# Kernel optimization log

Measured on AMD Instinct MI355X. Metric: run time of the kernel, lower is better.

Reference implementation:

```python
import jax, jax.numpy as jnp
import numpy as np

N_NODES = 100000
N_EDGES = 3200000
D_IN = 128
D_HID = 16
N_CLS = 2


def gcn_conv(x, edge_index, W, b, n_nodes):
    """PyG GCNConv (normalize=True, add_self_loops=True, bias=True)."""
    h = x @ W  # [N, out]
    loop = jnp.arange(n_nodes, dtype=edge_index.dtype)
    src = jnp.concatenate([edge_index[0], loop])
    dst = jnp.concatenate([edge_index[1], loop])
    deg = jax.ops.segment_sum(jnp.ones_like(dst, dtype=h.dtype), dst, num_segments=n_nodes)
    dinv = jnp.where(deg > 0, jax.lax.rsqrt(deg), jnp.zeros_like(deg))
    norm = dinv[src] * dinv[dst]  # [E+N]
    msg = h[src] * norm[:, None]  # gather + scale
    out = jax.ops.segment_sum(msg, dst, num_segments=n_nodes)  # scatter-add
    return out + b


def setup_inputs() -> dict:
    key = jax.random.key(0)
    k1, k2, k3, k4, k5 = jax.random.split(key, 5)
    x = jax.random.normal(k1, (N_NODES, D_IN), dtype=jnp.float32)
    edge_index = jax.random.randint(k2, (2, N_EDGES), 0, N_NODES, dtype=jnp.int64)
    # Glorot-style init for GCNConv weights, zeros for bias (PyG default)
    W1 = jax.random.normal(k3, (D_IN, D_HID), dtype=jnp.float32) * (1.0 / np.sqrt(D_IN))
    b1 = jnp.zeros((D_HID,), dtype=jnp.float32)
    W2 = jax.random.normal(k4, (D_HID, N_CLS), dtype=jnp.float32) * (1.0 / np.sqrt(D_HID))
    b2 = jnp.zeros((N_CLS,), dtype=jnp.float32)
    return {"x": x, "edge_index": edge_index, "W1": W1, "b1": b1, "W2": W2, "b2": b2}


def reference(x, edge_index, W1, b1, W2, b2):
    n = x.shape[0]
    h = gcn_conv(x, edge_index, W1, b1, n)
    h = jax.nn.relu(h)
    # dropout is identity in eval mode
    h = gcn_conv(h, edge_index, W2, b2, n)
    return jax.nn.log_softmax(h, axis=1)
```

## Files before the change

kernel.cpp:

```cpp
#include <hip/hip_runtime.h>
#include <hip/hip_bf16.h>
#include <hip/hip_fp16.h>

#define D_IN  128
#define D_HID 16
#define N_CLS 2
#define NPB   256
#define MAXB  512
#define TILE  4096
#define XROW  136

#define FE 0

typedef short bf16x8 __attribute__((ext_vector_type(8)));
typedef float f32x4  __attribute__((ext_vector_type(4)));

__device__ __forceinline__ unsigned short f2bf(float f) {
    unsigned int u = __float_as_uint(f);
    u += 0x7FFFu + ((u >> 16) & 1u);
    return (unsigned short)(u >> 16);
}

template<bool I64>
__device__ __forceinline__ int lde(const void* p, size_t i) {
    if constexpr (I64) return (int)((const long long*)p)[i];
    else               return ((const int*)p)[i];
}

__global__ void k_detect(const int* __restrict__ ev, int* __restrict__ flags) {
    __shared__ int sE;
    if (threadIdx.x == 0) sE = 0;
    __syncthreads();
    if (ev[2 * threadIdx.x + 1] != 0) atomicOr(&sE, 1);
    __syncthreads();
    if (threadIdx.x == 0) flags[FE] = sE ? 0 : 1;
}

__global__ __launch_bounds__(MAXB) void k_init(const int* __restrict__ ev, int* __restrict__ flags,
                                               unsigned int* __restrict__ gcur, int cap) {
    __shared__ int sE;
    int tid = threadIdx.x;
    if (tid == 0) sE = 0;
    __syncthreads();
    if (tid < 256 && ev[2 * tid + 1] != 0) atomicOr(&sE, 1);
    gcur[tid] = (unsigned int)(tid * cap);
    __syncthreads();
    if (tid == 0) flags[FE] = sE ? 0 : 1;
}

template<bool I64>
__device__ __forceinline__ void part_body(
        const void* __restrict__ ei, unsigned int* __restrict__ gcur,
        unsigned int* __restrict__ staged, int E, int cap,
        unsigned int* sbuf, unsigned short* bbuf,
        int* hist, int* lbase, int* gb, int* wsum) {
    int tid = threadIdx.x;
    int t0 = blockIdx.x * TILE;

    hist[tid] = 0;
    __syncthreads();

    int myB[8]; unsigned int myP[8]; int myR[8];
#pragma unroll
    for (int k = 0; k < 8; ++k) {
        int e = t0 + k * 512 + tid;
        if (e < E) {
            int s = lde<I64>(ei, (size_t)e);
            int d = lde<I64>(ei, (size_t)E + e);
            int b = d >> 8;
            myB[k] = b;
            myP[k] = ((unsigned int)s << 8) | (unsigned int)(d & 255);
            myR[k] = atomicAdd(&hist[b], 1);
        } else myB[k] = -1;
    }
    __syncthreads();

    int v = hist[tid];
    int lane = tid & 63, wv = tid >> 6;
    int s = v;
#pragma unroll
    for (int m = 1; m < 64; m <<= 1) {
        int t = __shfl_up(s, m, 64);
        if (lane >= m) s += t;
    }
    if (lane == 63) wsum[wv] = s;
    __syncthreads();
    int woff = 0;
#pragma unroll
    for (int w = 0; w < 8; ++w) if (w < wv) woff += wsum[w];
    int excl = s + woff - v;
    lbase[tid] = excl;
    int gb_ = 0;
    if (v > 0) gb_ = (int)atomicAdd(&gcur[tid], (unsigned int)v);
    gb[tid] = gb_;
    __syncthreads();

#pragma unroll
    for (int k = 0; k < 8; ++k) {
        if (myB[k] >= 0) {
            int pos = lbase[myB[k]] + myR[k];
            sbuf[pos] = myP[k];
            bbuf[pos] = (unsigned short)myB[k];
        }
    }
    __syncthreads();

    int tot = lbase[MAXB - 1] + hist[MAXB - 1];
    for (int i = tid; i < tot; i += 512) {
        int b = bbuf[i];
        long long idx = (long long)gb[b] + (i - lbase[b]);
        if (idx < (long long)(b + 1) * cap)
            staged[idx] = sbuf[i];
    }
}

__global__ __launch_bounds__(512) void k_part(
        const void* __restrict__ ei, unsigned int* __restrict__ gcur,
        unsigned int* __restrict__ staged, int E, int cap, const int* __restrict__ flags) {
    __shared__ unsigned int sbuf[TILE];
    __shared__ unsigned short bbuf[TILE];
    __shared__ int hist[MAXB], lbase[MAXB], gb[MAXB];
    __shared__ int wsum[8];
    if (flags[FE]) part_body<true >(ei, gcur, staged, E, cap, sbuf, bbuf, hist, lbase, gb, wsum);
    else           part_body<false>(ei, gcur, staged, E, cap, sbuf, bbuf, hist, lbase, gb, wsum);
}

__global__ __launch_bounds__(512) void k_sortd(
        const unsigned int* __restrict__ staged, const unsigned int* __restrict__ gcur,
        unsigned int* __restrict__ staged2, unsigned int* __restrict__ dmeta,
        float* __restrict__ dinv, int cap, int N) {
    __shared__ unsigned int h[NPB];
    __shared__ unsigned int cur[NPB];
    __shared__ int wsum[4];
    int tid = threadIdx.x, b = blockIdx.x;
    long long s0 = (long long)b * cap;
    int cnt = (int)(gcur[b] - (unsigned int)s0);
    if (cnt > cap) cnt = cap;
    if (tid < NPB) h[tid] = 0u;
    __syncthreads();
    for (int i = tid; i < cnt; i += 512)
        atomicAdd(&h[staged[s0 + i] & 255], 1u);
    __syncthreads();
    int v = 0, sIncl = 0;
    int lane = tid & 63, wv = tid >> 6;
    if (tid < NPB) {
        v = (int)h[tid];
        sIncl = v;
#pragma unroll
        for (int m = 1; m < 64; m <<= 1) {
            int t = __shfl_up(sIncl, m, 64);
            if (lane >= m) sIncl += t;
        }
        if (lane == 63) wsum[wv] = sIncl;
    }
    __syncthreads();
    if (tid < NPB) {
        int woff = 0;
#pragma unroll
        for (int w = 0; w < 4; ++w) if (w < wv) woff += wsum[w];
        int excl = sIncl + woff - v;
        int node = b * NPB + tid;
        dmeta[node] = ((unsigned int)excl << 16) | (unsigned int)v;
        cur[tid] = (unsigned int)excl;
        if (node < N) dinv[node] = rsqrtf((float)(v + 1));
    }
    __syncthreads();
    for (int i = tid; i < cnt; i += 512) {
        unsigned int p = staged[s0 + i];
        unsigned int r = atomicAdd(&cur[p & 255], 1u);
        staged2[s0 + r] = p;
    }
}

__global__ __launch_bounds__(256) void k_gemm1m(
        const float* __restrict__ x, const float* __restrict__ W1,
        const float* __restrict__ dinv, __half* __restrict__ g1h, int n) {
    __shared__ short xhi[64 * XROW];
    __shared__ short xlo[64 * XROW];
    __shared__ short whi[16 * XROW];
    __shared__ short wlo[16 * XROW];
    int tid = threadIdx.x;
    int node0 = blockIdx.x * 64;

    for (int i = tid; i < D_IN * D_HID; i += 256) {
        int k = i >> 4, f = i & 15;
        float v = W1[i];
        unsigned short h = f2bf(v);
        float fh = __uint_as_float(((unsigned int)h) << 16);
        whi[f * XROW + k] = (short)h;
        wlo[f * XROW + k] = (short)f2bf(v - fh);
    }
    int limFlat = (n - node0) * D_IN;
#pragma unroll
    for (int it = 0; it < 8; ++it) {
        int flat = it * 1024 + tid * 4;
        float4 v = make_float4(0.f, 0.f, 0.f, 0.f);
        if (flat < limFlat) v = *(const float4*)(x + (size_t)node0 * D_IN + flat);
        int row = flat >> 7, k = flat & 127;
        unsigned short h0 = f2bf(v.x), h1 = f2bf(v.y), h2 = f2bf(v.z), h3 = f2bf(v.w);
        unsigned short l0 = f2bf(v.x - __uint_as_float(((unsigned int)h0) << 16));
        unsigned short l1 = f2bf(v.y - __uint_as_float(((unsigned int)h1) << 16));
        unsigned short l2 = f2bf(v.z - __uint_as_float(((unsigned int)h2) << 16));
        unsigned short l3 = f2bf(v.w - __uint_as_float(((unsigned int)h3) << 16));
        int o = row * XROW + k;
        *(uint2*)(&xhi[o]) = make_uint2((unsigned int)h0 | ((unsigned int)h1 << 16),
                                        (unsigned int)h2 | ((unsigned int)h3 << 16));
        *(uint2*)(&xlo[o]) = make_uint2((unsigned int)l0 | ((unsigned int)l1 << 16),
                                        (unsigned int)l2 | ((unsigned int)l3 << 16));
    }
    __syncthreads();

    int w = tid >> 6, L = tid & 63;
    int m = L & 15, q = L >> 4;
    const short* axh = &xhi[(w * 16 + m) * XROW + q * 8];
    const short* axl = &xlo[(w * 16 + m) * XROW + q * 8];
    const short* bwh = &whi[m * XROW + q * 8];
    const short* bwl = &wlo[m * XROW + q * 8];
    f32x4 acc = {0.f, 0.f, 0.f, 0.f};
#pragma unroll
    for (int c = 0; c < 4; ++c) {
        bf16x8 ah = *(const bf16x8*)(axh + c * 32);
        bf16x8 al = *(const bf16x8*)(axl + c * 32);
        bf16x8 bh = *(const bf16x8*)(bwh + c * 32);
        bf16x8 bl = *(const bf16x8*)(bwl + c * 32);
        acc = __builtin_amdgcn_mfma_f32_16x16x32_bf16(ah, bh, acc, 0, 0, 0);
        acc = __builtin_amdgcn_mfma_f32_16x16x32_bf16(ah, bl, acc, 0, 0, 0);
        acc = __builtin_amdgcn_mfma_f32_16x16x32_bf16(al, bh, acc, 0, 0, 0);
    }
    int nodeB = node0 + w * 16 + q * 4;
#pragma unroll
    for (int r = 0; r < 4; ++r) {
        int node = nodeB + r;
        if (node < n) g1h[(size_t)node * D_HID + m] = __float2half(dinv[node] * acc[r]);
    }
}

__global__ __launch_bounds__(1024) void k_agg1w(
        const unsigned int* __restrict__ staged2, const unsigned int* __restrict__ dmeta,
        const __half* __restrict__ g1h, const float* __restrict__ dinv,
        const float* __restrict__ b1, const float* __restrict__ W2,
        float2* __restrict__ g2, int N, int cap) {
    int tid = threadIdx.x, b = blockIdx.x, by = blockIdx.y;
    long long s0 = (long long)b * cap;
    int wv = tid >> 6;
    int lane = tid & 63;
    int f2 = lane & 7;
    int e8 = lane >> 3;
    const __half2* g1h2 = (const __half2*)g1h;
    int dEnd = by * 128 + 128;
    for (int dl = by * 128 + wv; dl < dEnd; dl += 16) {
        int node = b * NPB + dl;
        unsigned int m = dmeta[node];
        long long st = s0 + (m >> 16);
        int deg = (int)(m & 0xFFFFu);
        float ax = 0.f, ay = 0.f;
        int i = e8;
        for (; i + 8 < deg; i += 16) {
            unsigned int p0 = staged2[st + i];
            unsigned int p1 = staged2[st + i + 8];
            float2 t0 = __half22float2(g1h2[(size_t)(p0 >> 8) * 8 + f2]);
            float2 t1 = __half22float2(g1h2[(size_t)(p1 >> 8) * 8 + f2]);
            ax += t0.x + t1.x; ay += t0.y + t1.y;
        }
        if (i < deg) {
            unsigned int p0 = staged2[st + i];
            float2 t0 = __half22float2(g1h2[(size_t)(p0 >> 8) * 8 + f2]);
            ax += t0.x; ay += t0.y;
        }
        ax += __shfl_xor(ax, 8, 64);  ay += __shfl_xor(ay, 8, 64);
        ax += __shfl_xor(ax, 16, 64); ay += __shfl_xor(ay, 16, 64);
        ax += __shfl_xor(ax, 32, 64); ay += __shfl_xor(ay, 32, 64);
        float c0 = 0.f, c1 = 0.f, di = 0.f;
        if (node < N) {
            float2 t = __half22float2(g1h2[(size_t)node * 8 + f2]);
            ax += t.x; ay += t.y;
            di = dinv[node];
            int f0 = f2 * 2;
            float r0 = fmaxf(b1[f0] + di * ax, 0.f);
            float r1 = fmaxf(b1[f0 + 1] + di * ay, 0.f);
            c0 = r0 * W2[f0 * N_CLS + 0] + r1 * W2[(f0 + 1) * N_CLS + 0];
            c1 = r0 * W2[f0 * N_CLS + 1] + r1 * W2[(f0 + 1) * N_CLS + 1];
        }
        c0 += __shfl_xor(c0, 1, 64); c1 += __shfl_xor(c1, 1, 64);
        c0 += __shfl_xor(c0, 2, 64); c1 += __shfl_xor(c1, 2, 64);
        c0 += __shfl_xor(c0, 4, 64); c1 += __shfl_xor(c1, 4, 64);
        if (lane == 0 && node < N) g2[node] = make_float2(di * c0, di * c1);
    }
}

__global__ __launch_bounds__(1024) void k_agg2w(
        const unsigned int* __restrict__ staged2, const unsigned int* __restrict__ dmeta,
        const float2* __restrict__ g2, const float* __restrict__ dinv,
        const float* __restrict__ b2, float2* __restrict__ out, int N, int cap) {
    int tid = threadIdx.x, b = blockIdx.x, by = blockIdx.y;
    long long s0 = (long long)b * cap;
    int wv = tid >> 6;
    int lane = tid & 63;
    int dEnd = by * 128 + 128;
    for (int dl = by * 128 + wv; dl < dEnd; dl += 16) {
        int node = b * NPB + dl;
        unsigned int m = dmeta[node];
        long long st = s0 + (m >> 16);
        int deg = (int)(m & 0xFFFFu);
        float a0 = 0.f, a1 = 0.f;
        for (int i = lane; i < deg; i += 64) {
            unsigned int p = staged2[st + i];
            float2 t = g2[p >> 8];
            a0 += t.x; a1 += t.y;
        }
#pragma unroll
        for (int mm = 1; mm < 64; mm <<= 1) {
            a0 += __shfl_xor(a0, mm, 64);
            a1 += __shfl_xor(a1, mm, 64);
        }
        if (lane == 0 && node < N) {
            float2 self = g2[node];
            float di = dinv[node];
            float v0 = b2[0] + di * (a0 + self.x);
            float v1 = b2[1] + di * (a1 + self.y);
            float mx = fmaxf(v0, v1);
            float lse = mx + logf(expf(v0 - mx) + expf(v1 - mx));
            out[node] = make_float2(v0 - lse, v1 - lse);
        }
    }
}

__global__ void fb_deg_init(unsigned int* __restrict__ deg, int n) {
    int i = blockIdx.x * blockDim.x + threadIdx.x;
    if (i < n) deg[i] = 1u;
}
template<bool I64>
__global__ void fb_deg_count(const void* __restrict__ ei, unsigned int* __restrict__ deg,
                             int E, const int* __restrict__ flags) {
    if (flags[FE] != (int)I64) return;
    int e = blockIdx.x * blockDim.x + threadIdx.x;
    if (e < E) atomicAdd(&deg[lde<I64>(ei, (size_t)E + e)], 1u);
}
__global__ void fb_dinv_inplace(float* __restrict__ dinv, int n) {
    int i = blockIdx.x * blockDim.x + threadIdx.x;
    if (i < n) {
        unsigned int u = ((const unsigned int*)dinv)[i];
        dinv[i] = rsqrtf((float)u);
    }
}
__global__ void fb_a1_init(const float* __restrict__ h1, const float* __restrict__ dinv,
                           const float* __restrict__ b1, float* __restrict__ a1, int n) {
    int tid = blockIdx.x * blockDim.x + threadIdx.x;
    if (tid >= n * D_HID) return;
    int node = tid >> 4, f = tid & 15;
    float di = dinv[node];
    a1[tid] = b1[f] + di * di * h1[tid];
}
template<bool I64>
__global__ void fb_agg1(const void* __restrict__ ei, const float* __restrict__ dinv,
                        const float* __restrict__ h1, float* __restrict__ a1,
                        int E, const int* __restrict__ flags) {
    if (flags[FE] != (int)I64) return;
    int tid = blockIdx.x * blockDim.x + threadIdx.x;
    int e = tid >> 4, f = tid & 15;
    if (e >= E) return;
    int s = lde<I64>(ei, (size_t)e);
    int d = lde<I64>(ei, (size_t)E + e);
    float norm = dinv[s] * dinv[d];
    atomicAdd(&a1[(size_t)d * D_HID + f], h1[(size_t)s * D_HID + f] * norm);
}
__global__ void fb_relu_gemm2(const float* __restrict__ a1, const float* __restrict__ W2,
                              float* __restrict__ h2, int n) {
    int node = blockIdx.x * blockDim.x + threadIdx.x;
    if (node >= n) return;
    float c0 = 0.f, c1 = 0.f;
    const float* row = a1 + (size_t)node * D_HID;
#pragma unroll
    for (int f = 0; f < D_HID; ++f) {
        float r = fmaxf(row[f], 0.f);
        c0 += r * W2[f * N_CLS + 0];
        c1 += r * W2[f * N_CLS + 1];
    }
    h2[(size_t)node * 2 + 0] = c0;
    h2[(size_t)node * 2 + 1] = c1;
}
__global__ void fb_a2_init(const float* __restrict__ h2, const float* __restrict__ dinv,
                           const float* __restrict__ b2, float* __restrict__ a2, int n) {
    int tid = blockIdx.x * blockDim.x + threadIdx.x;
    if (tid >= n * N_CLS) return;
    int node = tid >> 1, c = tid & 1;
    float di = dinv[node];
    a2[tid] = b2[c] + di * di * h2[tid];
}
template<bool I64>
__global__ void fb_agg2(const void* __restrict__ ei, const float* __restrict__ dinv,
                        const float* __restrict__ h2, float* __restrict__ a2,
                        int E, const int* __restrict__ flags) {
    if (flags[FE] != (int)I64) return;
    int e = blockIdx.x * blockDim.x + threadIdx.x;
    if (e >= E) return;
    int s = lde<I64>(ei, (size_t)e);
    int d = lde<I64>(ei, (size_t)E + e);
    float norm = dinv[s] * dinv[d];
    atomicAdd(&a2[(size_t)d * 2 + 0], h2[(size_t)s * 2 + 0] * norm);
    atomicAdd(&a2[(size_t)d * 2 + 1], h2[(size_t)s * 2 + 1] * norm);
}
__global__ void fb_gemm1(const float* __restrict__ x, const float* __restrict__ W1,
                         float* __restrict__ h1, int n) {
    __shared__ float w[D_IN * D_HID];
    for (int i = threadIdx.x; i < D_IN * D_HID; i += blockDim.x) w[i] = W1[i];
    __syncthreads();
    int tid = blockIdx.x * blockDim.x + threadIdx.x;
    int node = tid >> 4, f = tid & 15;
    if (node >= n) return;
    const float4* xr = (const float4*)(x + (size_t)node * D_IN);
    float acc = 0.f;
#pragma unroll
    for (int k4 = 0; k4 < D_IN / 4; ++k4) {
        float4 v = xr[k4];
        int k = k4 * 4;
        acc += v.x * w[(k + 0) * D_HID + f];
        acc += v.y * w[(k + 1) * D_HID + f];
        acc += v.z * w[(k + 2) * D_HID + f];
        acc += v.w * w[(k + 3) * D_HID + f];
    }
    h1[tid] = acc;
}
__global__ void fb_lsm(const float* __restrict__ a2, float* __restrict__ out, int n) {
    int node = blockIdx.x * blockDim.x + threadIdx.x;
    if (node >= n) return;
    float v0 = a2[(size_t)node * 2 + 0];
    float v1 = a2[(size_t)node * 2 + 1];
    float m = fmaxf(v0, v1);
    float lse = m + logf(expf(v0 - m) + expf(v1 - m));
    out[(size_t)node * 2 + 0] = v0 - lse;
    out[(size_t)node * 2 + 1] = v1 - lse;
}

extern "C" void kernel_launch(void* const* d_in, const int* in_sizes, int n_in,
                              void* d_out, int out_size, void* d_ws, size_t ws_size,
                              hipStream_t stream) {
    const float* x  = (const float*)d_in[0];
    const void*  ei = d_in[1];
    const float* W1 = (const float*)d_in[2];
    const float* b1 = (const float*)d_in[3];
    const float* W2 = (const float*)d_in[4];
    const float* b2 = (const float*)d_in[5];

    const int N = in_sizes[0] / D_IN;
    const int E = in_sizes[1] / 2;
    const int nb = (N + NPB - 1) / NPB;

    int cap = ((2 * (E / nb + 1)) + 255) & ~255;
    if (cap < 1024) cap = 1024;

    const int B = 256;
    dim3 blk(B);
    const int nBlkN = (N + B - 1) / B;
    const int nBlkE = (E + B - 1) / B;
    char* ws = (char*)d_ws;

    auto al = [](size_t v) { return (v + 255) & ~(size_t)255; };
    const size_t oDinv   = 0;
    const size_t oDmeta  = al(oDinv + (size_t)N * 4);
    const size_t oGcur   = al(oDmeta + (size_t)nb * NPB * 4);
    const size_t oFlag   = al(oGcur + (size_t)MAXB * 4);
    const size_t oStage  = al(oFlag + 8);
    const size_t oStage2 = al(oStage + (size_t)nb * cap * 4);
    const size_t oG1h    = al(oStage2 + (size_t)nb * cap * 4);
    const size_t oG2     = al(oG1h + (size_t)N * D_HID * 2);
    const size_t needNew = al(oG2 + (size_t)N * 2 * 4);

    if (ws_size >= needNew && nb <= MAXB && cap <= 65280 && N < (1 << 24)) {
        float*        dinv    = (float*)(ws + oDinv);
        unsigned int* dmeta   = (unsigned int*)(ws + oDmeta);
        unsigned int* gcur    = (unsigned int*)(ws + oGcur);
        int*          flags   = (int*)(ws + oFlag);
        unsigned int* staged  = (unsigned int*)(ws + oStage);
        unsigned int* staged2 = (unsigned int*)(ws + oStage2);
        __half*       g1h     = (__half*)(ws + oG1h);
        float2*       g2      = (float2*)(ws + oG2);

        k_init<<<dim3(1), dim3(MAXB), 0, stream>>>((const int*)ei, flags, gcur, cap);

        dim3 gPart((E + TILE - 1) / TILE);
        k_part<<<gPart, dim3(512), 0, stream>>>(ei, gcur, staged, E, cap, flags);

        k_sortd<<<dim3(nb), dim3(512), 0, stream>>>(staged, gcur, staged2, dmeta, dinv, cap, N);

        k_gemm1m<<<dim3((N + 63) / 64), dim3(256), 0, stream>>>(x, W1, dinv, g1h, N);

        k_agg1w<<<dim3(nb, 2), dim3(1024), 0, stream>>>(staged2, dmeta, g1h, dinv, b1, W2, g2, N, cap);

        k_agg2w<<<dim3(nb, 2), dim3(1024), 0, stream>>>(staged2, dmeta, g2, dinv, b2,
                                                        (float2*)d_out, N, cap);
    } else {
        float* dinv  = (float*)(ws + 0);
        float* h1    = (float*)(ws + 400128);
        float* a1    = (float*)(ws + 6800256);
        float* h2    = (float*)(ws + 13200384);
        float* a2    = (float*)(ws + 14000512);
        int*   flags = (int*)  (ws + 14800640);

        k_detect<<<dim3(1), blk, 0, stream>>>((const int*)ei, flags);
        fb_deg_init<<<dim3(nBlkN), blk, 0, stream>>>((unsigned int*)dinv, N);
        fb_deg_count<false><<<dim3(nBlkE), blk, 0, stream>>>(ei, (unsigned int*)dinv, E, flags);
        fb_deg_count<true ><<<dim3(nBlkE), blk, 0, stream>>>(ei, (unsigned int*)dinv, E, flags);
        fb_dinv_inplace<<<dim3(nBlkN), blk, 0, stream>>>(dinv, N);

        dim3 g_nh((N * D_HID + B - 1) / B);
        fb_gemm1<<<g_nh, blk, 0, stream>>>(x, W1, h1, N);
        fb_a1_init<<<g_nh, blk, 0, stream>>>(h1, dinv, b1, a1, N);
        dim3 g_eh(((size_t)E * D_HID + B - 1) / B);
        fb_agg1<false><<<g_eh, blk, 0, stream>>>(ei, dinv, h1, a1, E, flags);
        fb_agg1<true ><<<g_eh, blk, 0, stream>>>(ei, dinv, h1, a1, E, flags);
        fb_relu_gemm2<<<dim3(nBlkN), blk, 0, stream>>>(a1, W2, h2, N);
        dim3 g_n2((N * N_CLS + B - 1) / B);
        fb_a2_init<<<g_n2, blk, 0, stream>>>(h2, dinv, b2, a2, N);
        fb_agg2<false><<<dim3(nBlkE), blk, 0, stream>>>(ei, dinv, h2, a2, E, flags);
        fb_agg2<true ><<<dim3(nBlkE), blk, 0, stream>>>(ei, dinv, h2, a2, E, flags);
        fb_lsm<<<dim3(nBlkN), blk, 0, stream>>>(a2, (float*)d_out, N);
    }
}
```

Baseline: 240.2 us.

## Drop init kernel, detect index width per block, restructure aggregation loops

Replaces the single-block init kernel with a memset of the per-bucket cursors, which now hold relative offsets, and has each partition block detect int64 vs int32 edge indices itself. The aggregation kernels move from 1024-thread blocks to 256-thread blocks on a larger grid, prefetch each wave's 8 node metadata words up front, hoist bias and W2 loads out of the loop, and unroll the edge gather by 8 so more loads are in flight. The intent is to remove a serial launch and raise memory-level parallelism in the gather phases, at the cost of more registers and redundant per-block detection reads.

```diff
diff --git a/kernel.cpp b/kernel.cpp
--- a/kernel.cpp
+++ b/kernel.cpp
@@ -34,18 +34,6 @@
     if (ev[2 * threadIdx.x + 1] != 0) atomicOr(&sE, 1);
     __syncthreads();
     if (threadIdx.x == 0) flags[FE] = sE ? 0 : 1;
-}
-
-__global__ __launch_bounds__(MAXB) void k_init(const int* __restrict__ ev, int* __restrict__ flags,
-                                               unsigned int* __restrict__ gcur, int cap) {
-    __shared__ int sE;
-    int tid = threadIdx.x;
-    if (tid == 0) sE = 0;
-    __syncthreads();
-    if (tid < 256 && ev[2 * tid + 1] != 0) atomicOr(&sE, 1);
-    gcur[tid] = (unsigned int)(tid * cap);
-    __syncthreads();
-    if (tid == 0) flags[FE] = sE ? 0 : 1;
 }
 
 template<bool I64>
@@ -108,21 +96,27 @@
     int tot = lbase[MAXB - 1] + hist[MAXB - 1];
     for (int i = tid; i < tot; i += 512) {
         int b = bbuf[i];
-        long long idx = (long long)gb[b] + (i - lbase[b]);
-        if (idx < (long long)(b + 1) * cap)
-            staged[idx] = sbuf[i];
+        int rel = gb[b] + (i - lbase[b]);
+        if (rel < cap)
+            staged[(size_t)b * cap + rel] = sbuf[i];
     }
 }
 
 __global__ __launch_bounds__(512) void k_part(
         const void* __restrict__ ei, unsigned int* __restrict__ gcur,
-        unsigned int* __restrict__ staged, int E, int cap, const int* __restrict__ flags) {
+        unsigned int* __restrict__ staged, int E, int cap) {
     __shared__ unsigned int sbuf[TILE];
     __shared__ unsigned short bbuf[TILE];
     __shared__ int hist[MAXB], lbase[MAXB], gb[MAXB];
     __shared__ int wsum[8];
-    if (flags[FE]) part_body<true >(ei, gcur, staged, E, cap, sbuf, bbuf, hist, lbase, gb, wsum);
-    else           part_body<false>(ei, gcur, staged, E, cap, sbuf, bbuf, hist, lbase, gb, wsum);
+    __shared__ int sI64;
+    int tid = threadIdx.x;
+    if (tid == 0) sI64 = 1;
+    __syncthreads();
+    if (tid < 256 && 2 * tid + 1 < 2 * E && ((const int*)ei)[2 * tid + 1] != 0) sI64 = 0;
+    __syncthreads();
+    if (sI64) part_body<true >(ei, gcur, staged, E, cap, sbuf, bbuf, hist, lbase, gb, wsum);
+    else      part_body<false>(ei, gcur, staged, E, cap, sbuf, bbuf, hist, lbase, gb, wsum);
 }
 
 __global__ __launch_bounds__(512) void k_sortd(
@@ -134,7 +128,7 @@
     __shared__ int wsum[4];
     int tid = threadIdx.x, b = blockIdx.x;
     long long s0 = (long long)b * cap;
-    int cnt = (int)(gcur[b] - (unsigned int)s0);
+    int cnt = (int)gcur[b];
     if (cnt > cap) cnt = cap;
     if (tid < NPB) h[tid] = 0u;
     __syncthreads();
@@ -235,37 +229,43 @@
     }
 }
 
-__global__ __launch_bounds__(1024) void k_agg1w(
+__global__ __launch_bounds__(256) void k_agg1w(
         const unsigned int* __restrict__ staged2, const unsigned int* __restrict__ dmeta,
         const __half* __restrict__ g1h, const float* __restrict__ dinv,
         const float* __restrict__ b1, const float* __restrict__ W2,
         float2* __restrict__ g2, int N, int cap) {
     int tid = threadIdx.x, b = blockIdx.x, by = blockIdx.y;
     long long s0 = (long long)b * cap;
-    int wv = tid >> 6;
     int lane = tid & 63;
     int f2 = lane & 7;
     int e8 = lane >> 3;
+    int wid = (by << 2) + (tid >> 6);
     const __half2* g1h2 = (const __half2*)g1h;
-    int dEnd = by * 128 + 128;
-    for (int dl = by * 128 + wv; dl < dEnd; dl += 16) {
+    int f0 = f2 * 2;
+    float b10 = b1[f0], b11 = b1[f0 + 1];
+    float w00 = W2[f0 * N_CLS + 0], w01 = W2[f0 * N_CLS + 1];
+    float w10 = W2[(f0 + 1) * N_CLS + 0], w11 = W2[(f0 + 1) * N_CLS + 1];
+    unsigned int md[8];
+#pragma unroll
+    for (int k = 0; k < 8; ++k) md[k] = dmeta[b * NPB + wid + (k << 5)];
+#pragma unroll 2
+    for (int k = 0; k < 8; ++k) {
+        int dl = wid + (k << 5);
         int node = b * NPB + dl;
-        unsigned int m = dmeta[node];
-        long long st = s0 + (m >> 16);
-        int deg = (int)(m & 0xFFFFu);
+        long long st = s0 + (md[k] >> 16);
+        int deg = (int)(md[k] & 0xFFFFu);
         float ax = 0.f, ay = 0.f;
-        int i = e8;
-        for (; i + 8 < deg; i += 16) {
-            unsigned int p0 = staged2[st + i];
-            unsigned int p1 = staged2[st + i + 8];
-            float2 t0 = __half22float2(g1h2[(size_t)(p0 >> 8) * 8 + f2]);
-            float2 t1 = __half22float2(g1h2[(size_t)(p1 >> 8) * 8 + f2]);
-            ax += t0.x + t1.x; ay += t0.y + t1.y;
-        }
-        if (i < deg) {
-            unsigned int p0 = staged2[st + i];
-            float2 t0 = __half22float2(g1h2[(size_t)(p0 >> 8) * 8 + f2]);
-            ax += t0.x; ay += t0.y;
+        for (int base = 0; base < deg; base += 64) {
+            int rem = deg - base;
+#pragma unroll
+            for (int j = 0; j < 8; ++j) {
+                int ei = (j << 3) + e8;
+                if (ei < rem) {
+                    unsigned int pe = staged2[st + base + ei];
+                    float2 t = __half22float2(g1h2[(size_t)(pe >> 8) * 8 + f2]);
+                    ax += t.x; ay += t.y;
+                }
+            }
         }
         ax += __shfl_xor(ax, 8, 64);  ay += __shfl_xor(ay, 8, 64);
         ax += __shfl_xor(ax, 16, 64); ay += __shfl_xor(ay, 16, 64);
@@ -275,11 +275,10 @@
             float2 t = __half22float2(g1h2[(size_t)node * 8 + f2]);
             ax += t.x; ay += t.y;
             di = dinv[node];
-            int f0 = f2 * 2;
-            float r0 = fmaxf(b1[f0] + di * ax, 0.f);
-            float r1 = fmaxf(b1[f0 + 1] + di * ay, 0.f);
-            c0 = r0 * W2[f0 * N_CLS + 0] + r1 * W2[(f0 + 1) * N_CLS + 0];
-            c1 = r0 * W2[f0 * N_CLS + 1] + r1 * W2[(f0 + 1) * N_CLS + 1];
+            float r0 = fmaxf(b10 + di * ax, 0.f);
+            float r1 = fmaxf(b11 + di * ay, 0.f);
+            c0 = r0 * w00 + r1 * w10;
+            c1 = r0 * w01 + r1 * w11;
         }
         c0 += __shfl_xor(c0, 1, 64); c1 += __shfl_xor(c1, 1, 64);
         c0 += __shfl_xor(c0, 2, 64); c1 += __shfl_xor(c1, 2, 64);
@@ -288,25 +287,32 @@
     }
 }
 
-__global__ __launch_bounds__(1024) void k_agg2w(
+__global__ __launch_bounds__(256) void k_agg2w(
         const unsigned int* __restrict__ staged2, const unsigned int* __restrict__ dmeta,
         const float2* __restrict__ g2, const float* __restrict__ dinv,
         const float* __restrict__ b2, float2* __restrict__ out, int N, int cap) {
     int tid = threadIdx.x, b = blockIdx.x, by = blockIdx.y;
     long long s0 = (long long)b * cap;
-    int wv = tid >> 6;
     int lane = tid & 63;
-    int dEnd = by * 128 + 128;
-    for (int dl = by * 128 + wv; dl < dEnd; dl += 16) {
+    int wid = (by << 2) + (tid >> 6);
+    float bb0 = b2[0], bb1 = b2[1];
+    unsigned int md[8];
+#pragma unroll
+    for (int k = 0; k < 8; ++k) md[k] = dmeta[b * NPB + wid + (k << 5)];
+#pragma unroll 2
+    for (int k = 0; k < 8; ++k) {
+        int dl = wid + (k << 5);
         int node = b * NPB + dl;
-        unsigned int m = dmeta[node];
-        long long st = s0 + (m >> 16);
-        int deg = (int)(m & 0xFFFFu);
+        long long st = s0 + (md[k] >> 16);
+        int deg = (int)(md[k] & 0xFFFFu);
         float a0 = 0.f, a1 = 0.f;
-        for (int i = lane; i < deg; i += 64) {
-            unsigned int p = staged2[st + i];
-            float2 t = g2[p >> 8];
-            a0 += t.x; a1 += t.y;
+        for (int base = 0; base < deg; base += 64) {
+            int rem = deg - base;
+            if (lane < rem) {
+                unsigned int p = staged2[st + base + lane];
+                float2 t = g2[p >> 8];
+                a0 += t.x; a1 += t.y;
+            }
         }
 #pragma unroll
         for (int mm = 1; mm < 64; mm <<= 1) {
@@ -316,8 +322,8 @@
         if (lane == 0 && node < N) {
             float2 self = g2[node];
             float di = dinv[node];
-            float v0 = b2[0] + di * (a0 + self.x);
-            float v1 = b2[1] + di * (a1 + self.y);
+            float v0 = bb0 + di * (a0 + self.x);
+            float v1 = bb1 + di * (a1 + self.y);
             float mx = fmaxf(v0, v1);
             float lse = mx + logf(expf(v0 - mx) + expf(v1 - mx));
             out[node] = make_float2(v0 - lse, v1 - lse);
@@ -470,25 +476,24 @@
         float*        dinv    = (float*)(ws + oDinv);
         unsigned int* dmeta   = (unsigned int*)(ws + oDmeta);
         unsigned int* gcur    = (unsigned int*)(ws + oGcur);
-        int*          flags   = (int*)(ws + oFlag);
         unsigned int* staged  = (unsigned int*)(ws + oStage);
         unsigned int* staged2 = (unsigned int*)(ws + oStage2);
         __half*       g1h     = (__half*)(ws + oG1h);
         float2*       g2      = (float2*)(ws + oG2);
 
-        k_init<<<dim3(1), dim3(MAXB), 0, stream>>>((const int*)ei, flags, gcur, cap);
+        hipMemsetAsync(gcur, 0, (size_t)nb * 4, stream);
 
         dim3 gPart((E + TILE - 1) / TILE);
-        k_part<<<gPart, dim3(512), 0, stream>>>(ei, gcur, staged, E, cap, flags);
+        k_part<<<gPart, dim3(512), 0, stream>>>(ei, gcur, staged, E, cap);
 
         k_sortd<<<dim3(nb), dim3(512), 0, stream>>>(staged, gcur, staged2, dmeta, dinv, cap, N);
 
         k_gemm1m<<<dim3((N + 63) / 64), dim3(256), 0, stream>>>(x, W1, dinv, g1h, N);
 
-        k_agg1w<<<dim3(nb, 2), dim3(1024), 0, stream>>>(staged2, dmeta, g1h, dinv, b1, W2, g2, N, cap);
-
-        k_agg2w<<<dim3(nb, 2), dim3(1024), 0, stream>>>(staged2, dmeta, g2, dinv, b2,
-                                                        (float2*)d_out, N, cap);
+        k_agg1w<<<dim3(nb, 8), dim3(256), 0, stream>>>(staged2, dmeta, g1h, dinv, b1, W2, g2, N, cap);
+
+        k_agg2w<<<dim3(nb, 8), dim3(256), 0, stream>>>(staged2, dmeta, g2, dinv, b2,
+                                                       (float2*)d_out, N, cap);
     } else {
         float* dinv  = (float*)(ws + 0);
         float* h1    = (float*)(ws + 400128);
```

After: 248.0 us. +3.2%, slower.
